# Performance work log

Measured on AMD Instinct MI355X. Metric: run time of the kernel, lower is better.

Reference implementation:

```python
import jax, jax.numpy as jnp
import numpy as np

N, M, D = 62, 512, 256  # parts, batch samples (P*K = 64*8), hidden dim
K_PER_ID = 8
MARGIN = 0.2


def setup_inputs() -> dict:
    key = jax.random.key(0)
    k1, = jax.random.split(key, 1)
    feature = jax.random.normal(k1, (N, M, D), dtype=jnp.float32)
    # P*K structured labels (uniform class sizes are REQUIRED by the original
    # masked_select(...).view(n, m, -1) reshape): 64 ids, 8 samples each,
    # identical label layout for every part row n.
    row = jnp.arange(M, dtype=jnp.int64) // K_PER_ID  # [M]
    label = jnp.tile(row[None, :], (N, 1))            # [N, M]
    return {"feature": feature, "label": label}


def _safe_sqrt(x):
    # sqrt(relu(x)) with a zero (finite) gradient at x <= 0, matching the
    # forward values of torch.sqrt(F.relu(x)) exactly.
    pos = x > 0
    return jnp.where(pos, jnp.sqrt(jnp.where(pos, x, 1.0)), 0.0)


def reference(feature, label):
    # feature: [n, m, d], label: [n, m]
    sq = jnp.sum(feature * feature, axis=2)                       # [n, m]
    gram = jnp.einsum('nmd,nkd->nmk', feature, feature)           # [n, m, m]
    d2 = sq[:, :, None] + sq[:, None, :] - 2.0 * gram             # [n, m, m]
    dist = _safe_sqrt(jnp.maximum(d2, 0.0))                       # [n, m, m]

    dist_mean = jnp.mean(dist, axis=(1, 2))                       # [n]

    pos_mask = label[:, :, None] == label[:, None, :]             # [n, m, m]
    # hard positive: max dist over same-label columns (incl. self)
    hard_hp = jnp.max(jnp.where(pos_mask, dist, -jnp.inf), axis=2)   # [n, m]
    # hard negative: min dist over different-label columns
    hard_hn = jnp.min(jnp.where(pos_mask, jnp.inf, dist), axis=2)    # [n, m]

    hard_loss = jax.nn.relu(MARGIN + hard_hp - hard_hn)           # [n, m]
    hard_loss_mean = jnp.mean(hard_loss, axis=1)                  # [n]
    return hard_loss_mean, dist_mean
```

## Files before the change

kernel.cpp:

```cpp
#include <hip/hip_runtime.h>

#define N_PARTS 62
#define M_SAMP  512
#define D_DIM   256
#define MARGIN  0.2f
#define ROWS    (N_PARTS * M_SAMP)
#define PART_ELEMS (M_SAMP * D_DIM)

typedef unsigned short ushort_t;
typedef __attribute__((ext_vector_type(8))) short bf16x8;
typedef __attribute__((ext_vector_type(4))) float f32x4;

__device__ __forceinline__ ushort_t bf16_rne(float f) {
    unsigned u = __float_as_uint(f);
    unsigned r = u + 0x7fffu + ((u >> 16) & 1u);
    return (ushort_t)(r >> 16);
}

__global__ __launch_bounds__(256) void prep_kernel(const float* __restrict__ feat,
                                                   ushort_t* __restrict__ Fb,
                                                   float* __restrict__ sq,
                                                   float* __restrict__ out) {
    const int id = blockIdx.x;
    const int n  = id & 63;
    const int rb = id >> 6;
    if (id == 0 && threadIdx.x < 2 * N_PARTS) out[threadIdx.x] = 0.0f;
    if (n >= N_PARTS) return;
    const int wv   = threadIdx.x >> 6;
    const int lane = threadIdx.x & 63;
    const int rp   = rb * 4 + wv;
    const int row  = n * M_SAMP + rp;
    const float4 v = ((const float4*)(feat + (size_t)row * D_DIM))[lane];
    ushort4 us;
    us.x = bf16_rne(v.x); us.y = bf16_rne(v.y);
    us.z = bf16_rne(v.z); us.w = bf16_rne(v.w);
    const float fx = __uint_as_float((unsigned)us.x << 16);
    const float fy = __uint_as_float((unsigned)us.y << 16);
    const float fz = __uint_as_float((unsigned)us.z << 16);
    const float fw = __uint_as_float((unsigned)us.w << 16);
    const int c  = lane >> 3;
    const int q  = (lane >> 1) & 3;
    const int g  = rp >> 4;
    const int fl = (rp & 15) | (q << 4);
    *(ushort4*)(Fb + (size_t)n * PART_ELEMS + ((size_t)(c * 32 + g) * 512)
                + fl * 8 + (lane & 1) * 4) = us;
    float ssum = fx * fx + fy * fy + fz * fz + fw * fw;
    #pragma unroll
    for (int off = 32; off > 0; off >>= 1) ssum += __shfl_xor(ssum, off);
    if (lane == 0) sq[row] = ssum;
}

__global__ __launch_bounds__(512, 2) void fused_triplet_kernel(const ushort_t* __restrict__ Fb,
                                                               const float* __restrict__ sq,
                                                               float* __restrict__ out) {
    const int id = blockIdx.x;
    const int n  = id & 63;
    const int ct = id >> 6;
    if (n >= N_PARTS) return;
    const int tid = threadIdx.x;
    const int wave = tid >> 6, lane = tid & 63;
    const ushort_t* F = Fb + (size_t)n * PART_ELEMS;
    const float* SQ = sq + n * M_SAMP;

    __shared__ float mrg[8][128][3];

    const ushort_t* aptr = F + (size_t)(wave * 4) * 512 + lane * 8;
    const ushort_t* bptr = F + (size_t)(ct * 8) * 512 + lane * 8;

    f32x4 acc[4][8] = {};

    #pragma unroll
    for (int c = 0; c < 8; ++c) {
        const size_t off = (size_t)c * (32 * 512);
        bf16x8 af[4], bf[8];
        #pragma unroll
        for (int i = 0; i < 4; ++i)
            af[i] = *(const bf16x8*)(aptr + off + (size_t)i * 512);
        #pragma unroll
        for (int i = 0; i < 8; ++i)
            bf[i] = *(const bf16x8*)(bptr + off + (size_t)i * 512);
        #pragma unroll
        for (int mi = 0; mi < 4; ++mi)
            #pragma unroll
            for (int ni = 0; ni < 8; ++ni)
                acc[mi][ni] = __builtin_amdgcn_mfma_f32_16x16x32_bf16(
                    af[mi], bf[ni], acc[mi][ni], 0, 0, 0);
    }

    float sqr[4][4];
    #pragma unroll
    for (int mi = 0; mi < 4; ++mi)
        #pragma unroll
        for (int p = 0; p < 4; ++p)
            sqr[mi][p] = SQ[wave * 64 + mi * 16 + (lane >> 4) * 4 + p];

    #pragma unroll
    for (int ni = 0; ni < 8; ++ni) {
        const int C = ct * 128 + ni * 16 + (lane & 15);
        const float sc = SQ[C];
        const int Cg = C >> 3;
        float ds = 0.f, hp = 0.f, hn = 1e30f;
        #pragma unroll
        for (int mi = 0; mi < 4; ++mi) {
            #pragma unroll
            for (int p = 0; p < 4; ++p) {
                const int R = wave * 64 + mi * 16 + (lane >> 4) * 4 + p;
                const float d2 = sqr[mi][p] + sc - 2.f * acc[mi][ni][p];
                const float d  = __builtin_amdgcn_sqrtf(fmaxf(d2, 0.f));
                ds += d;
                if ((R >> 3) == Cg) hp = fmaxf(hp, d);
                else                hn = fminf(hn, d);
            }
        }
        #pragma unroll
        for (int off = 16; off < 64; off <<= 1) {
            ds += __shfl_xor(ds, off);
            hp = fmaxf(hp, __shfl_xor(hp, off));
            hn = fminf(hn, __shfl_xor(hn, off));
        }
        if (lane < 16) {
            mrg[wave][ni * 16 + lane][0] = hp;
            mrg[wave][ni * 16 + lane][1] = hn;
            mrg[wave][ni * 16 + lane][2] = ds;
        }
    }
    __syncthreads();
    if (tid < 128) {
        float hp = 0.f, hn = 1e30f, bd = 0.f;
        #pragma unroll
        for (int w = 0; w < 8; ++w) {
            hp = fmaxf(hp, mrg[w][tid][0]);
            hn = fminf(hn, mrg[w][tid][1]);
            bd += mrg[w][tid][2];
        }
        const float bl = fmaxf(MARGIN + hp - hn, 0.f);
        mrg[0][tid][0] = bl;
        mrg[0][tid][1] = bd;
    }
    __syncthreads();
    if (tid < 64) {
        float bl = mrg[0][tid][0] + mrg[0][tid + 64][0];
        float bd = mrg[0][tid][1] + mrg[0][tid + 64][1];
        #pragma unroll
        for (int off = 32; off > 0; off >>= 1) {
            bl += __shfl_xor(bl, off);
            bd += __shfl_xor(bd, off);
        }
        if (lane == 0) {
            atomicAdd(&out[n],           bl * (1.0f / 512.0f));
            atomicAdd(&out[N_PARTS + n], bd * (1.0f / (512.0f * 512.0f)));
        }
    }
}

extern "C" void kernel_launch(void* const* d_in, const int* in_sizes, int n_in,
                              void* d_out, int out_size, void* d_ws, size_t ws_size,
                              hipStream_t stream) {
    const float* feat = (const float*)d_in[0];
    float* out = (float*)d_out;

    ushort_t* Fb = (ushort_t*)d_ws;
    float* sq    = (float*)((char*)d_ws + (size_t)ROWS * D_DIM * 2);

    prep_kernel<<<dim3(128 * 64), 256, 0, stream>>>(feat, Fb, sq, out);
    fused_triplet_kernel<<<dim3(4 * 64), 512, 0, stream>>>(Fb, sq, out);
}
```

Before: 92.43 us.

## Fuse bf16 conversion and norms into triplet kernel with double-buffered LDS staging

Removes the separate prep kernel and its bf16 workspace round trip. Each block now loads fp32 features for its part directly, converts them to bf16, computes squared norms, and stages 32-wide K slices into a swizzled, double-buffered LDS tile. The next slice's global loads are overlapped with the MFMA work on the current one. In exchange, each of the 4 column-tile blocks per part redundantly reads and converts the full part's fp32 data (4x the global reads of fp32 versus bf16). LDS use grows to about 80KB per block, which may limit occupancy.

```diff
diff --git a/kernel.cpp b/kernel.cpp
--- a/kernel.cpp
+++ b/kernel.cpp
@@ -4,8 +4,6 @@
 #define M_SAMP  512
 #define D_DIM   256
 #define MARGIN  0.2f
-#define ROWS    (N_PARTS * M_SAMP)
-#define PART_ELEMS (M_SAMP * D_DIM)
 
 typedef unsigned short ushort_t;
 typedef __attribute__((ext_vector_type(8))) short bf16x8;
@@ -17,87 +15,115 @@
     return (ushort_t)(r >> 16);
 }
 
-__global__ __launch_bounds__(256) void prep_kernel(const float* __restrict__ feat,
-                                                   ushort_t* __restrict__ Fb,
-                                                   float* __restrict__ sq,
-                                                   float* __restrict__ out) {
-    const int id = blockIdx.x;
-    const int n  = id & 63;
-    const int rb = id >> 6;
-    if (id == 0 && threadIdx.x < 2 * N_PARTS) out[threadIdx.x] = 0.0f;
-    if (n >= N_PARTS) return;
-    const int wv   = threadIdx.x >> 6;
-    const int lane = threadIdx.x & 63;
-    const int rp   = rb * 4 + wv;
-    const int row  = n * M_SAMP + rp;
-    const float4 v = ((const float4*)(feat + (size_t)row * D_DIM))[lane];
-    ushort4 us;
-    us.x = bf16_rne(v.x); us.y = bf16_rne(v.y);
-    us.z = bf16_rne(v.z); us.w = bf16_rne(v.w);
-    const float fx = __uint_as_float((unsigned)us.x << 16);
-    const float fy = __uint_as_float((unsigned)us.y << 16);
-    const float fz = __uint_as_float((unsigned)us.z << 16);
-    const float fw = __uint_as_float((unsigned)us.w << 16);
-    const int c  = lane >> 3;
-    const int q  = (lane >> 1) & 3;
-    const int g  = rp >> 4;
-    const int fl = (rp & 15) | (q << 4);
-    *(ushort4*)(Fb + (size_t)n * PART_ELEMS + ((size_t)(c * 32 + g) * 512)
-                + fl * 8 + (lane & 1) * 4) = us;
-    float ssum = fx * fx + fy * fy + fz * fz + fw * fw;
-    #pragma unroll
-    for (int off = 32; off > 0; off >>= 1) ssum += __shfl_xor(ssum, off);
-    if (lane == 0) sq[row] = ssum;
+__device__ __forceinline__ int lds_off(int row, int q) {
+    return row * 32 + ((q ^ ((row >> 1) & 3)) << 3);
 }
 
-__global__ __launch_bounds__(512, 2) void fused_triplet_kernel(const ushort_t* __restrict__ Fb,
-                                                               const float* __restrict__ sq,
-                                                               float* __restrict__ out) {
+__global__ void zero_out_kernel(float* __restrict__ out) {
+    if (threadIdx.x < 2 * N_PARTS) out[threadIdx.x] = 0.0f;
+}
+
+__global__ __launch_bounds__(512, 2) void fused_all_kernel(
+        const float* __restrict__ feat, float* __restrict__ out) {
     const int id = blockIdx.x;
     const int n  = id & 63;
     const int ct = id >> 6;
     if (n >= N_PARTS) return;
-    const int tid = threadIdx.x;
+    const int tid  = threadIdx.x;
     const int wave = tid >> 6, lane = tid & 63;
-    const ushort_t* F = Fb + (size_t)n * PART_ELEMS;
-    const float* SQ = sq + n * M_SAMP;
 
+    __shared__ ushort_t tile[2][512 * 32];
+    __shared__ float sqA[M_SAMP];
     __shared__ float mrg[8][128][3];
 
-    const ushort_t* aptr = F + (size_t)(wave * 4) * 512 + lane * 8;
-    const ushort_t* bptr = F + (size_t)(ct * 8) * 512 + lane * 8;
+    const int r8 = tid >> 3;
+    const int k4 = tid & 7;
+    const float* fb = feat + (size_t)n * (M_SAMP * D_DIM) + (size_t)k4 * 4;
 
     f32x4 acc[4][8] = {};
+    float sqp[8] = {0.f, 0.f, 0.f, 0.f, 0.f, 0.f, 0.f, 0.f};
+
+    #pragma unroll
+    for (int i = 0; i < 8; ++i) {
+        const int row = i * 64 + r8;
+        const float4 v = *(const float4*)(fb + (size_t)row * D_DIM);
+        ushort4 us;
+        us.x = bf16_rne(v.x); us.y = bf16_rne(v.y);
+        us.z = bf16_rne(v.z); us.w = bf16_rne(v.w);
+        const float fx = __uint_as_float((unsigned)us.x << 16);
+        const float fy = __uint_as_float((unsigned)us.y << 16);
+        const float fz = __uint_as_float((unsigned)us.z << 16);
+        const float fw = __uint_as_float((unsigned)us.w << 16);
+        sqp[i] += fx * fx + fy * fy + fz * fz + fw * fw;
+        *(ushort4*)(&tile[0][lds_off(row, k4 >> 1) + (k4 & 1) * 4]) = us;
+    }
+    __syncthreads();
 
     #pragma unroll
     for (int c = 0; c < 8; ++c) {
-        const size_t off = (size_t)c * (32 * 512);
+        float4 nx[8];
+        if (c < 7) {
+            #pragma unroll
+            for (int i = 0; i < 8; ++i)
+                nx[i] = *(const float4*)(fb + (size_t)(i * 64 + r8) * D_DIM
+                                            + (size_t)(c + 1) * 32);
+        }
+        const ushort_t* tb = tile[c & 1];
         bf16x8 af[4], bf[8];
         #pragma unroll
         for (int i = 0; i < 4; ++i)
-            af[i] = *(const bf16x8*)(aptr + off + (size_t)i * 512);
+            af[i] = *(const bf16x8*)(tb + lds_off(wave * 64 + i * 16 + (lane & 15),
+                                                  lane >> 4));
         #pragma unroll
         for (int i = 0; i < 8; ++i)
-            bf[i] = *(const bf16x8*)(bptr + off + (size_t)i * 512);
+            bf[i] = *(const bf16x8*)(tb + lds_off(ct * 128 + i * 16 + (lane & 15),
+                                                  lane >> 4));
         #pragma unroll
         for (int mi = 0; mi < 4; ++mi)
             #pragma unroll
             for (int ni = 0; ni < 8; ++ni)
                 acc[mi][ni] = __builtin_amdgcn_mfma_f32_16x16x32_bf16(
                     af[mi], bf[ni], acc[mi][ni], 0, 0, 0);
+        if (c < 7) {
+            ushort_t* tn = tile[(c + 1) & 1];
+            #pragma unroll
+            for (int i = 0; i < 8; ++i) {
+                const int row = i * 64 + r8;
+                ushort4 us;
+                us.x = bf16_rne(nx[i].x); us.y = bf16_rne(nx[i].y);
+                us.z = bf16_rne(nx[i].z); us.w = bf16_rne(nx[i].w);
+                const float fx = __uint_as_float((unsigned)us.x << 16);
+                const float fy = __uint_as_float((unsigned)us.y << 16);
+                const float fz = __uint_as_float((unsigned)us.z << 16);
+                const float fw = __uint_as_float((unsigned)us.w << 16);
+                sqp[i] += fx * fx + fy * fy + fz * fz + fw * fw;
+                *(ushort4*)(&tn[lds_off(row, k4 >> 1) + (k4 & 1) * 4]) = us;
+            }
+        }
+        __syncthreads();
     }
+
+    #pragma unroll
+    for (int i = 0; i < 8; ++i) {
+        float s = sqp[i];
+        s += __shfl_xor(s, 1);
+        s += __shfl_xor(s, 2);
+        s += __shfl_xor(s, 4);
+        if (k4 == 0) sqA[i * 64 + r8] = s;
+    }
+    __syncthreads();
 
     float sqr[4][4];
     #pragma unroll
     for (int mi = 0; mi < 4; ++mi)
         #pragma unroll
         for (int p = 0; p < 4; ++p)
-            sqr[mi][p] = SQ[wave * 64 + mi * 16 + (lane >> 4) * 4 + p];
+            sqr[mi][p] = sqA[wave * 64 + mi * 16 + (lane >> 4) * 4 + p];
 
     #pragma unroll
     for (int ni = 0; ni < 8; ++ni) {
         const int C = ct * 128 + ni * 16 + (lane & 15);
-        const float sc = SQ[C];
+        const float sc = sqA[C];
         const int Cg = C >> 3;
         float ds = 0.f, hp = 0.f, hn = 1e30f;
         #pragma unroll
@@ -158,10 +184,8 @@
                               hipStream_t stream) {
     const float* feat = (const float*)d_in[0];
     float* out = (float*)d_out;
+    (void)d_ws; (void)ws_size;
 
-    ushort_t* Fb = (ushort_t*)d_ws;
-    float* sq    = (float*)((char*)d_ws + (size_t)ROWS * D_DIM * 2);
-
-    prep_kernel<<<dim3(128 * 64), 256, 0, stream>>>(feat, Fb, sq, out);
-    fused_triplet_kernel<<<dim3(4 * 64), 512, 0, stream>>>(Fb, sq, out);
+    zero_out_kernel<<<dim3(1), 128, 0, stream>>>(out);
+    fused_all_kernel<<<dim3(4 * 64), 512, 0, stream>>>(feat, out);
 }
```

Result: slower. 151.5 us (+63.9%).
